# Performance work log

Hardware: AMD Instinct MI355X
Metric: run time of the kernel (lower is better)

## Reference

```python
import jax, jax.numpy as jnp
import numpy as np

B, T, D, H, O, E = 4, 2048, 1024, 2048, 1024, 8
EPS = 1e-12  # torch F.normalize p=1 eps


def setup_inputs() -> dict:
    key = jax.random.key(0)
    ks = jax.random.split(key, 8)
    s = lambda *dims: 1.0 / np.sqrt(dims[0])
    return {
        "x": jax.random.normal(ks[0], (B, T, D), dtype=jnp.float32),
        "num_experts_chosen": 2,
        "W_gate": jax.random.normal(ks[1], (D, E), dtype=jnp.float32) * s(D),
        "b_gate": jnp.zeros((E,), dtype=jnp.float32),
        "W1": jax.random.normal(ks[2], (E, D, H), dtype=jnp.float32) * s(D),
        "b1": jnp.zeros((E, H), dtype=jnp.float32),
        "W2": jax.random.normal(ks[3], (E, H, O), dtype=jnp.float32) * s(H),
        "b2": jnp.zeros((E, O), dtype=jnp.float32),
    }


def reference(x, num_experts_chosen, W_gate, b_gate, W1, b1, W2, b2):
    # Router: softmax over experts -> [b, t, E]
    gating = jax.nn.softmax(jnp.einsum("btd,de->bte", x, W_gate) + b_gate, axis=-1)

    # Top-k mask (scatter of ones at top-k indices), then L1 renormalize
    _, topk_idx = jax.lax.top_k(gating, num_experts_chosen)  # [b, t, k]
    mask = jax.nn.one_hot(topk_idx, E, dtype=gating.dtype).sum(axis=-2)  # [b, t, E]
    g = gating * mask
    g = g / jnp.maximum(jnp.sum(jnp.abs(g), axis=-1, keepdims=True), EPS)

    # Dense compute of ALL experts (faithful to original), eval-mode dropout = identity
    h = jax.nn.relu(jnp.einsum("btd,edh->bteh", x, W1) + b1)  # [b, t, E, H]
    eo = jnp.einsum("bteh,eho->bteo", h, W2) + b2              # [b, t, E, O]

    # Weighted combine over experts
    return jnp.einsum("bte,bteo->bto", g, eo)
```

## Files before the change

kernel.cpp:

```cpp
#include <hip/hip_runtime.h>
#include <hip/hip_bf16.h>

typedef unsigned short u16;
typedef __attribute__((ext_vector_type(8))) short short8;
typedef __attribute__((ext_vector_type(4))) float floatx4;

#define NB 4
#define NT 2048
#define ND 1024
#define NH 2048
#define NO 1024
#define NE 8
#define NTOK (NB * NT)

#define BM 128
#define BN 128
#define BK 32

__device__ __forceinline__ u16 f2bf(float f) {
  __hip_bfloat16 h = __float2bfloat16(f);
  return *reinterpret_cast<u16*>(&h);
}

__device__ __forceinline__ float bf2f(unsigned u) {
  return __uint_as_float(u << 16);
}

__device__ __forceinline__ void async16(const u16* g, u16* l) {
  __builtin_amdgcn_global_load_lds(
      (const __attribute__((address_space(1))) void*)g,
      (__attribute__((address_space(3))) void*)l, 16, 0, 0);
}

__global__ __launch_bounds__(256) void transpose_cvt(
    const float* __restrict__ in, u16* __restrict__ out, int R, int C) {
  __shared__ float tile[64][65];
  int e = blockIdx.z;
  in  += (size_t)e * R * C;
  out += (size_t)e * R * C;
  int c0 = blockIdx.x * 64, r0 = blockIdx.y * 64;
  int t = threadIdx.x;
#pragma unroll
  for (int i = 0; i < 4; ++i) {
    int idx = t + i * 256;
    int r = idx >> 4, cq = idx & 15;
    float4 v = *(const float4*)&in[(size_t)(r0 + r) * C + c0 + cq * 4];
    tile[r][cq * 4 + 0] = v.x; tile[r][cq * 4 + 1] = v.y;
    tile[r][cq * 4 + 2] = v.z; tile[r][cq * 4 + 3] = v.w;
  }
  __syncthreads();
#pragma unroll
  for (int i = 0; i < 4; ++i) {
    int idx = t + i * 256;
    int c = idx >> 4, rq = idx & 15;
    uint2 p;
    p.x = (unsigned)f2bf(tile[rq * 4 + 0][c]) | ((unsigned)f2bf(tile[rq * 4 + 1][c]) << 16);
    p.y = (unsigned)f2bf(tile[rq * 4 + 2][c]) | ((unsigned)f2bf(tile[rq * 4 + 3][c]) << 16);
    *(uint2*)&out[(size_t)(c0 + c) * R + r0 + rq * 4] = p;
  }
}

__global__ __launch_bounds__(256) void router_kernel(
    const float* __restrict__ x, const float* __restrict__ Wg,
    const float* __restrict__ bg, u16* __restrict__ xbf,
    int* __restrict__ counts, int* __restrict__ entries,
    float* __restrict__ wts) {
  int t = threadIdx.x;
  int tok = blockIdx.x * 16 + (t >> 4);
  int l16 = t & 15;

  float acc[8] = {};
  const float* xrow = x + (size_t)tok * ND;
  u16* xbrow = xbf + (size_t)tok * ND;
#pragma unroll
  for (int i = 0; i < 16; ++i) {
    int d0 = l16 * 4 + i * 64;
    float4 xv = *(const float4*)&xrow[d0];
    uint2 p;
    p.x = (unsigned)f2bf(xv.x) | ((unsigned)f2bf(xv.y) << 16);
    p.y = (unsigned)f2bf(xv.z) | ((unsigned)f2bf(xv.w) << 16);
    *(uint2*)&xbrow[d0] = p;
    const float* wr = Wg + (size_t)d0 * NE;
#pragma unroll
    for (int j = 0; j < 4; ++j) {
      float xs = (j == 0) ? xv.x : (j == 1) ? xv.y : (j == 2) ? xv.z : xv.w;
      float4 w0 = *(const float4*)&wr[j * NE];
      float4 w1 = *(const float4*)&wr[j * NE + 4];
      acc[0] += xs * w0.x; acc[1] += xs * w0.y;
      acc[2] += xs * w0.z; acc[3] += xs * w0.w;
      acc[4] += xs * w1.x; acc[5] += xs * w1.y;
      acc[6] += xs * w1.z; acc[7] += xs * w1.w;
    }
  }
#pragma unroll
  for (int off = 8; off; off >>= 1)
#pragma unroll
    for (int k = 0; k < 8; ++k) acc[k] += __shfl_down(acc[k], off, 16);

  if (l16 == 0) {
    float best = -1e30f, second = -1e30f;
    int e0 = 0, e1 = 0;
#pragma unroll
    for (int i = 0; i < NE; ++i) {
      float L = acc[i] + bg[i];
      if (L > best) { second = best; e1 = e0; best = L; e0 = i; }
      else if (L > second) { second = L; e1 = i; }
    }
    float p1 = __expf(second - best);
    float inv = 1.f / (1.f + p1);
    int pos0 = atomicAdd(&counts[e0], 1);
    entries[e0 * NTOK + pos0] = tok * 2;      wts[e0 * NTOK + pos0] = inv;
    int pos1 = atomicAdd(&counts[e1], 1);
    entries[e1 * NTOK + pos1] = tok * 2 + 1;  wts[e1 * NTOK + pos1] = p1 * inv;
  }
}

__global__ __launch_bounds__(256) void gemm1_kernel(
    const u16* __restrict__ xbf, const u16* __restrict__ w1t,
    const float* __restrict__ b1, const int* __restrict__ counts,
    const int* __restrict__ entries, u16* __restrict__ hbuf) {
  int b = blockIdx.x;
  int e = b & 7;
  int r = b >> 3;
  int m0 = (r >> 4) * BM;
  int n0 = (r & 15) * BN;
  int cnt = counts[e];
  if (m0 >= cnt) return;
  int rem = cnt - m0; if (rem > BM) rem = BM;

  __shared__ u16 As[BM * BK];
  __shared__ u16 Bs[BN * BK];
  __shared__ int ent_s[BM];

  int t = threadIdx.x;
  if (t < BM) ent_s[t] = (t < rem) ? entries[e * NTOK + m0 + t] : entries[e * NTOK];
  __syncthreads();

  int lane = t & 63, wv = t >> 6;
  int r0s = wv * 32 + (lane >> 2);
  int r1s = r0s + 16;
  int pg0 = ((lane & 3) ^ (r0s & 3)) * 8;
  int pg1 = ((lane & 3) ^ (r1s & 3)) * 8;
  const u16* gA0 = xbf + (size_t)(ent_s[r0s] >> 1) * ND + pg0;
  const u16* gA1 = xbf + (size_t)(ent_s[r1s] >> 1) * ND + pg1;
  const u16* Bbase = w1t + (size_t)e * NH * ND + (size_t)n0 * ND;
  const u16* gB0 = Bbase + (size_t)r0s * ND + pg0;
  const u16* gB1 = Bbase + (size_t)r1s * ND + pg1;
  u16* lA0 = As + (wv * 32) * BK;
  u16* lA1 = As + (wv * 32 + 16) * BK;
  u16* lB0 = Bs + (wv * 32) * BK;
  u16* lB1 = Bs + (wv * 32 + 16) * BK;

  int waveM = (wv >> 1) * 64, waveN = (wv & 1) * 64;
  int rA = lane & 15, quad = lane >> 4;
  int xq = (quad ^ (rA & 3)) * 8;
  const short8* aP[4]; const short8* bP[4];
#pragma unroll
  for (int i = 0; i < 4; ++i) {
    aP[i] = (const short8*)&As[(waveM + i * 16 + rA) * BK + xq];
    bP[i] = (const short8*)&Bs[(waveN + i * 16 + rA) * BK + xq];
  }

  floatx4 acc[4][4] = {};
  for (int k0 = 0; k0 < ND; k0 += BK) {
    async16(gA0 + k0, lA0);
    async16(gA1 + k0, lA1);
    async16(gB0 + k0, lB0);
    async16(gB1 + k0, lB1);
    __syncthreads();
    short8 a[4], b[4];
#pragma unroll
    for (int i = 0; i < 4; ++i) { a[i] = *aP[i]; b[i] = *bP[i]; }
#pragma unroll
    for (int i = 0; i < 4; ++i)
#pragma unroll
      for (int j = 0; j < 4; ++j)
        acc[i][j] = __builtin_amdgcn_mfma_f32_16x16x32_bf16(a[i], b[j], acc[i][j], 0, 0, 0);
    __syncthreads();
  }

#pragma unroll
  for (int i = 0; i < 4; ++i)
#pragma unroll
    for (int rr = 0; rr < 4; ++rr) {
      int lm = waveM + i * 16 + quad * 4 + rr;
      if (lm >= rem) continue;
      int ent = ent_s[lm];
      u16* dst = hbuf + (size_t)ent * NH + n0;
#pragma unroll
      for (int j = 0; j < 4; ++j) {
        int col = waveN + j * 16 + rA;
        float v = acc[i][j][rr] + b1[e * NH + n0 + col];
        dst[col] = f2bf(fmaxf(v, 0.f));
      }
    }
}

__global__ __launch_bounds__(256) void gemm2_kernel(
    const u16* __restrict__ hbuf, const u16* __restrict__ w2t,
    const float* __restrict__ b2, const int* __restrict__ counts,
    const int* __restrict__ entries, const float* __restrict__ wts,
    u16* __restrict__ eo) {
  int b = blockIdx.x;
  int e = b & 7;
  int r = b >> 3;
  int m0 = (r >> 3) * BM;
  int n0 = (r & 7) * BN;
  int cnt = counts[e];
  if (m0 >= cnt) return;
  int rem = cnt - m0; if (rem > BM) rem = BM;

  __shared__ u16 As[BM * BK];
  __shared__ u16 Bs[BN * BK];
  __shared__ int ent_s[BM];
  __shared__ float w_s[BM];

  int t = threadIdx.x;
  if (t < BM) {
    int src = (t < rem) ? (e * NTOK + m0 + t) : (e * NTOK);
    ent_s[t] = entries[src];
    w_s[t] = wts[src];
  }
  __syncthreads();

  int lane = t & 63, wv = t >> 6;
  int r0s = wv * 32 + (lane >> 2);
  int r1s = r0s + 16;
  int pg0 = ((lane & 3) ^ (r0s & 3)) * 8;
  int pg1 = ((lane & 3) ^ (r1s & 3)) * 8;
  const u16* gA0 = hbuf + (size_t)ent_s[r0s] * NH + pg0;
  const u16* gA1 = hbuf + (size_t)ent_s[r1s] * NH + pg1;
  const u16* Bbase = w2t + (size_t)e * NO * NH + (size_t)n0 * NH;
  const u16* gB0 = Bbase + (size_t)r0s * NH + pg0;
  const u16* gB1 = Bbase + (size_t)r1s * NH + pg1;
  u16* lA0 = As + (wv * 32) * BK;
  u16* lA1 = As + (wv * 32 + 16) * BK;
  u16* lB0 = Bs + (wv * 32) * BK;
  u16* lB1 = Bs + (wv * 32 + 16) * BK;

  int waveM = (wv >> 1) * 64, waveN = (wv & 1) * 64;
  int rA = lane & 15, quad = lane >> 4;
  int xq = (quad ^ (rA & 3)) * 8;
  const short8* aP[4]; const short8* bP[4];
#pragma unroll
  for (int i = 0; i < 4; ++i) {
    aP[i] = (const short8*)&As[(waveM + i * 16 + rA) * BK + xq];
    bP[i] = (const short8*)&Bs[(waveN + i * 16 + rA) * BK + xq];
  }

  floatx4 acc[4][4] = {};
  for (int k0 = 0; k0 < NH; k0 += BK) {
    async16(gA0 + k0, lA0);
    async16(gA1 + k0, lA1);
    async16(gB0 + k0, lB0);
    async16(gB1 + k0, lB1);
    __syncthreads();
    short8 a[4], b[4];
#pragma unroll
    for (int i = 0; i < 4; ++i) { a[i] = *aP[i]; b[i] = *bP[i]; }
#pragma unroll
    for (int i = 0; i < 4; ++i)
#pragma unroll
      for (int j = 0; j < 4; ++j)
        acc[i][j] = __builtin_amdgcn_mfma_f32_16x16x32_bf16(a[i], b[j], acc[i][j], 0, 0, 0);
    __syncthreads();
  }

#pragma unroll
  for (int i = 0; i < 4; ++i)
#pragma unroll
    for (int rr = 0; rr < 4; ++rr) {
      int lm = waveM + i * 16 + quad * 4 + rr;
      if (lm >= rem) continue;
      int ent = ent_s[lm];
      float w = w_s[lm];
      u16* dst = eo + (size_t)ent * NO + n0;
#pragma unroll
      for (int j = 0; j < 4; ++j) {
        int col = waveN + j * 16 + rA;
        float v = (acc[i][j][rr] + b2[e * NO + n0 + col]) * w;
        dst[col] = f2bf(v);
      }
    }
}

__global__ __launch_bounds__(256) void combine_kernel(
    const u16* __restrict__ eo, float* __restrict__ out) {
  size_t idx = (size_t)blockIdx.x * 256 + threadIdx.x;
  size_t tok = idx >> 8;
  int oq = (int)(idx & 255) * 4;
  const u16* p0 = eo + (tok * 2) * NO + oq;
  const u16* p1 = p0 + NO;
  uint2 ua = *(const uint2*)p0;
  uint2 ub = *(const uint2*)p1;
  float4 o;
  o.x = bf2f(ua.x & 0xffff) + bf2f(ub.x & 0xffff);
  o.y = bf2f(ua.x >> 16)    + bf2f(ub.x >> 16);
  o.z = bf2f(ua.y & 0xffff) + bf2f(ub.y & 0xffff);
  o.w = bf2f(ua.y >> 16)    + bf2f(ub.y >> 16);
  *(float4*)&out[tok * NO + oq] = o;
}

extern "C" void kernel_launch(void* const* d_in, const int* in_sizes, int n_in,
                              void* d_out, int out_size, void* d_ws, size_t ws_size,
                              hipStream_t stream) {
  (void)in_sizes; (void)n_in; (void)out_size; (void)ws_size;
  const float* x  = (const float*)d_in[0];
  const float* Wg = (const float*)d_in[2];
  const float* bg = (const float*)d_in[3];
  const float* W1 = (const float*)d_in[4];
  const float* b1 = (const float*)d_in[5];
  const float* W2 = (const float*)d_in[6];
  const float* b2 = (const float*)d_in[7];
  float* out = (float*)d_out;

  char* ws = (char*)d_ws;
  size_t off = 0;
  int*   counts  = (int*)(ws + off);   off += 256;
  int*   entries = (int*)(ws + off);   off += (size_t)NE * NTOK * 4;
  float* wts     = (float*)(ws + off); off += (size_t)NE * NTOK * 4;
  u16*   xbf     = (u16*)(ws + off);   off += (size_t)NTOK * ND * 2;
  u16*   w1t     = (u16*)(ws + off);   off += (size_t)NE * NH * ND * 2;
  u16*   w2t     = (u16*)(ws + off);   off += (size_t)NE * NO * NH * 2;
  u16*   hbuf    = (u16*)(ws + off);   off += (size_t)NTOK * 2 * NH * 2;
  u16*   eo      = w1t;

  hipMemsetAsync(counts, 0, 256, stream);

  transpose_cvt<<<dim3(NH / 64, ND / 64, NE), 256, 0, stream>>>(W1, w1t, ND, NH);
  transpose_cvt<<<dim3(NO / 64, NH / 64, NE), 256, 0, stream>>>(W2, w2t, NH, NO);
  router_kernel<<<NTOK / 16, 256, 0, stream>>>(x, Wg, bg, xbf, counts, entries, wts);
  gemm1_kernel<<<NE * (NTOK / BM) * (NH / BN), 256, 0, stream>>>(xbf, w1t, b1, counts, entries, hbuf);
  gemm2_kernel<<<NE * (NTOK / BM) * (NO / BN), 256, 0, stream>>>(hbuf, w2t, b2, counts, entries, wts, eo);
  combine_kernel<<<(NTOK * NO / 4) / 256, 256, 0, stream>>>(eo, out);
}
```

Measured before the change: 487.3 us.

## Double GEMM K-tile with 8-way swizzle and batch router atomics per block

Raises the K tile of both expert GEMMs from 32 to 64, using an 8-chunk XOR swizzle for LDS staging and issuing two MFMA k-steps per barrier pair. This halves the number of barriers and global-to-LDS rounds per output tile, at the cost of twice the shared memory per block. The router now handles 32 tokens per block and aggregates expert assignments in shared memory. It then does one atomicAdd per expert per block on counters padded to separate cache lines, which cuts atomic contention in exchange for serial writes by 8 threads.

```diff
diff --git a/kernel.cpp b/kernel.cpp
--- a/kernel.cpp
+++ b/kernel.cpp
@@ -15,7 +15,7 @@
 
 #define BM 128
 #define BN 128
-#define BK 32
+#define BK 64
 
 __device__ __forceinline__ u16 f2bf(float f) {
   __hip_bfloat16 h = __float2bfloat16(f);
@@ -65,16 +65,19 @@
     const float* __restrict__ bg, u16* __restrict__ xbf,
     int* __restrict__ counts, int* __restrict__ entries,
     float* __restrict__ wts) {
+  __shared__ int   se0[32], se1[32];
+  __shared__ float sw0[32], sw1[32];
   int t = threadIdx.x;
-  int tok = blockIdx.x * 16 + (t >> 4);
-  int l16 = t & 15;
-
-  float acc[8] = {};
+  int tl = t >> 3;
+  int l8 = t & 7;
+  int tok = blockIdx.x * 32 + tl;
+
   const float* xrow = x + (size_t)tok * ND;
   u16* xbrow = xbf + (size_t)tok * ND;
-#pragma unroll
-  for (int i = 0; i < 16; ++i) {
-    int d0 = l16 * 4 + i * 64;
+  float acc[8] = {};
+#pragma unroll 4
+  for (int i = 0; i < 32; ++i) {
+    int d0 = l8 * 4 + i * 32;
     float4 xv = *(const float4*)&xrow[d0];
     uint2 p;
     p.x = (unsigned)f2bf(xv.x) | ((unsigned)f2bf(xv.y) << 16);
@@ -93,11 +96,11 @@
     }
   }
 #pragma unroll
-  for (int off = 8; off; off >>= 1)
-#pragma unroll
-    for (int k = 0; k < 8; ++k) acc[k] += __shfl_down(acc[k], off, 16);
-
-  if (l16 == 0) {
+  for (int off = 4; off; off >>= 1)
+#pragma unroll
+    for (int k = 0; k < 8; ++k) acc[k] += __shfl_down(acc[k], off, 8);
+
+  if (l8 == 0) {
     float best = -1e30f, second = -1e30f;
     int e0 = 0, e1 = 0;
 #pragma unroll
@@ -108,10 +111,22 @@
     }
     float p1 = __expf(second - best);
     float inv = 1.f / (1.f + p1);
-    int pos0 = atomicAdd(&counts[e0], 1);
-    entries[e0 * NTOK + pos0] = tok * 2;      wts[e0 * NTOK + pos0] = inv;
-    int pos1 = atomicAdd(&counts[e1], 1);
-    entries[e1 * NTOK + pos1] = tok * 2 + 1;  wts[e1 * NTOK + pos1] = p1 * inv;
+    se0[tl] = e0; se1[tl] = e1;
+    sw0[tl] = inv; sw1[tl] = p1 * inv;
+  }
+  __syncthreads();
+
+  if (t < NE) {
+    int e = t;
+    int c = 0;
+#pragma unroll
+    for (int k = 0; k < 32; ++k) c += (se0[k] == e) + (se1[k] == e);
+    int pos = atomicAdd(&counts[e * 32], c);
+    int base = blockIdx.x * 32;
+    for (int k = 0; k < 32; ++k) {
+      if (se0[k] == e) { entries[e * NTOK + pos] = (base + k) * 2;     wts[e * NTOK + pos] = sw0[k]; ++pos; }
+      if (se1[k] == e) { entries[e * NTOK + pos] = (base + k) * 2 + 1; wts[e * NTOK + pos] = sw1[k]; ++pos; }
+    }
   }
 }
 
@@ -124,7 +139,7 @@
   int r = b >> 3;
   int m0 = (r >> 4) * BM;
   int n0 = (r & 15) * BN;
-  int cnt = counts[e];
+  int cnt = counts[e * 32];
   if (m0 >= cnt) return;
   int rem = cnt - m0; if (rem > BM) rem = BM;
 
@@ -137,45 +152,53 @@
   __syncthreads();
 
   int lane = t & 63, wv = t >> 6;
-  int r0s = wv * 32 + (lane >> 2);
-  int r1s = r0s + 16;
-  int pg0 = ((lane & 3) ^ (r0s & 3)) * 8;
-  int pg1 = ((lane & 3) ^ (r1s & 3)) * 8;
-  const u16* gA0 = xbf + (size_t)(ent_s[r0s] >> 1) * ND + pg0;
-  const u16* gA1 = xbf + (size_t)(ent_s[r1s] >> 1) * ND + pg1;
+  int srow = lane >> 3;
+  int schunk = lane & 7;
+  int pg = (schunk ^ srow) * 8;
+
   const u16* Bbase = w1t + (size_t)e * NH * ND + (size_t)n0 * ND;
-  const u16* gB0 = Bbase + (size_t)r0s * ND + pg0;
-  const u16* gB1 = Bbase + (size_t)r1s * ND + pg1;
-  u16* lA0 = As + (wv * 32) * BK;
-  u16* lA1 = As + (wv * 32 + 16) * BK;
-  u16* lB0 = Bs + (wv * 32) * BK;
-  u16* lB1 = Bs + (wv * 32 + 16) * BK;
+  const u16* gA[4]; const u16* gB[4];
+  u16 *lA[4], *lB[4];
+#pragma unroll
+  for (int j = 0; j < 4; ++j) {
+    int rr = wv * 32 + j * 8 + srow;
+    gA[j] = xbf + (size_t)(ent_s[rr] >> 1) * ND + pg;
+    gB[j] = Bbase + (size_t)rr * ND + pg;
+    lA[j] = As + (wv * 32 + j * 8) * BK;
+    lB[j] = Bs + (wv * 32 + j * 8) * BK;
+  }
 
   int waveM = (wv >> 1) * 64, waveN = (wv & 1) * 64;
   int rA = lane & 15, quad = lane >> 4;
-  int xq = (quad ^ (rA & 3)) * 8;
-  const short8* aP[4]; const short8* bP[4];
-#pragma unroll
-  for (int i = 0; i < 4; ++i) {
-    aP[i] = (const short8*)&As[(waveM + i * 16 + rA) * BK + xq];
-    bP[i] = (const short8*)&Bs[(waveN + i * 16 + rA) * BK + xq];
-  }
+  const short8* aP[2][4]; const short8* bP[2][4];
+#pragma unroll
+  for (int kk = 0; kk < 2; ++kk)
+#pragma unroll
+    for (int i = 0; i < 4; ++i) {
+      int cA = ((kk * 4 + quad) ^ (rA & 7)) * 8;
+      aP[kk][i] = (const short8*)&As[(waveM + i * 16 + rA) * BK + cA];
+      bP[kk][i] = (const short8*)&Bs[(waveN + i * 16 + rA) * BK + cA];
+    }
 
   floatx4 acc[4][4] = {};
   for (int k0 = 0; k0 < ND; k0 += BK) {
-    async16(gA0 + k0, lA0);
-    async16(gA1 + k0, lA1);
-    async16(gB0 + k0, lB0);
-    async16(gB1 + k0, lB1);
+#pragma unroll
+    for (int j = 0; j < 4; ++j) async16(gA[j] + k0, lA[j]);
+#pragma unroll
+    for (int j = 0; j < 4; ++j) async16(gB[j] + k0, lB[j]);
     __syncthreads();
-    short8 a[4], b[4];
-#pragma unroll
-    for (int i = 0; i < 4; ++i) { a[i] = *aP[i]; b[i] = *bP[i]; }
-#pragma unroll
-    for (int i = 0; i < 4; ++i)
-#pragma unroll
-      for (int j = 0; j < 4; ++j)
-        acc[i][j] = __builtin_amdgcn_mfma_f32_16x16x32_bf16(a[i], b[j], acc[i][j], 0, 0, 0);
+    short8 a[2][4], bb[2][4];
+#pragma unroll
+    for (int kk = 0; kk < 2; ++kk)
+#pragma unroll
+      for (int i = 0; i < 4; ++i) { a[kk][i] = *aP[kk][i]; bb[kk][i] = *bP[kk][i]; }
+#pragma unroll
+    for (int kk = 0; kk < 2; ++kk)
+#pragma unroll
+      for (int i = 0; i < 4; ++i)
+#pragma unroll
+        for (int j = 0; j < 4; ++j)
+          acc[i][j] = __builtin_amdgcn_mfma_f32_16x16x32_bf16(a[kk][i], bb[kk][j], acc[i][j], 0, 0, 0);
     __syncthreads();
   }
 
@@ -206,7 +229,7 @@
   int r = b >> 3;
   int m0 = (r >> 3) * BM;
   int n0 = (r & 7) * BN;
-  int cnt = counts[e];
+  int cnt = counts[e * 32];
   if (m0 >= cnt) return;
   int rem = cnt - m0; if (rem > BM) rem = BM;
 
@@ -224,45 +247,53 @@
   __syncthreads();
 
   int lane = t & 63, wv = t >> 6;
-  int r0s = wv * 32 + (lane >> 2);
-  int r1s = r0s + 16;
-  int pg0 = ((lane & 3) ^ (r0s & 3)) * 8;
-  int pg1 = ((lane & 3) ^ (r1s & 3)) * 8;
-  const u16* gA0 = hbuf + (size_t)ent_s[r0s] * NH + pg0;
-  const u16* gA1 = hbuf + (size_t)ent_s[r1s] * NH + pg1;
+  int srow = lane >> 3;
+  int schunk = lane & 7;
+  int pg = (schunk ^ srow) * 8;
+
   const u16* Bbase = w2t + (size_t)e * NO * NH + (size_t)n0 * NH;
-  const u16* gB0 = Bbase + (size_t)r0s * NH + pg0;
-  const u16* gB1 = Bbase + (size_t)r1s * NH + pg1;
-  u16* lA0 = As + (wv * 32) * BK;
-  u16* lA1 = As + (wv * 32 + 16) * BK;
-  u16* lB0 = Bs + (wv * 32) * BK;
-  u16* lB1 = Bs + (wv * 32 + 16) * BK;
+  const u16* gA[4]; const u16* gB[4];
+  u16 *lA[4], *lB[4];
+#pragma unroll
+  for (int j = 0; j < 4; ++j) {
+    int rr = wv * 32 + j * 8 + srow;
+    gA[j] = hbuf + (size_t)ent_s[rr] * NH + pg;
+    gB[j] = Bbase + (size_t)rr * NH + pg;
+    lA[j] = As + (wv * 32 + j * 8) * BK;
+    lB[j] = Bs + (wv * 32 + j * 8) * BK;
+  }
 
   int waveM = (wv >> 1) * 64, waveN = (wv & 1) * 64;
   int rA = lane & 15, quad = lane >> 4;
-  int xq = (quad ^ (rA & 3)) * 8;
-  const short8* aP[4]; const short8* bP[4];
-#pragma unroll
-  for (int i = 0; i < 4; ++i) {
-    aP[i] = (const short8*)&As[(waveM + i * 16 + rA) * BK + xq];
-    bP[i] = (const short8*)&Bs[(waveN + i * 16 + rA) * BK + xq];
-  }
+  const short8* aP[2][4]; const short8* bP[2][4];
+#pragma unroll
+  for (int kk = 0; kk < 2; ++kk)
+#pragma unroll
+    for (int i = 0; i < 4; ++i) {
+      int cA = ((kk * 4 + quad) ^ (rA & 7)) * 8;
+      aP[kk][i] = (const short8*)&As[(waveM + i * 16 + rA) * BK + cA];
+      bP[kk][i] = (const short8*)&Bs[(waveN + i * 16 + rA) * BK + cA];
+    }
 
   floatx4 acc[4][4] = {};
   for (int k0 = 0; k0 < NH; k0 += BK) {
-    async16(gA0 + k0, lA0);
-    async16(gA1 + k0, lA1);
-    async16(gB0 + k0, lB0);
-    async16(gB1 + k0, lB1);
+#pragma unroll
+    for (int j = 0; j < 4; ++j) async16(gA[j] + k0, lA[j]);
+#pragma unroll
+    for (int j = 0; j < 4; ++j) async16(gB[j] + k0, lB[j]);
     __syncthreads();
-    short8 a[4], b[4];
-#pragma unroll
-    for (int i = 0; i < 4; ++i) { a[i] = *aP[i]; b[i] = *bP[i]; }
-#pragma unroll
-    for (int i = 0; i < 4; ++i)
-#pragma unroll
-      for (int j = 0; j < 4; ++j)
-        acc[i][j] = __builtin_amdgcn_mfma_f32_16x16x32_bf16(a[i], b[j], acc[i][j], 0, 0, 0);
+    short8 a[2][4], bb[2][4];
+#pragma unroll
+    for (int kk = 0; kk < 2; ++kk)
+#pragma unroll
+      for (int i = 0; i < 4; ++i) { a[kk][i] = *aP[kk][i]; bb[kk][i] = *bP[kk][i]; }
+#pragma unroll
+    for (int kk = 0; kk < 2; ++kk)
+#pragma unroll
+      for (int i = 0; i < 4; ++i)
+#pragma unroll
+        for (int j = 0; j < 4; ++j)
+          acc[i][j] = __builtin_amdgcn_mfma_f32_16x16x32_bf16(a[kk][i], bb[kk][j], acc[i][j], 0, 0, 0);
     __syncthreads();
   }
 
@@ -316,7 +347,7 @@
 
   char* ws = (char*)d_ws;
   size_t off = 0;
-  int*   counts  = (int*)(ws + off);   off += 256;
+  int*   counts  = (int*)(ws + off);   off += NE * 32 * 4;
   int*   entries = (int*)(ws + off);   off += (size_t)NE * NTOK * 4;
   float* wts     = (float*)(ws + off); off += (size_t)NE * NTOK * 4;
   u16*   xbf     = (u16*)(ws + off);   off += (size_t)NTOK * ND * 2;
@@ -325,11 +356,11 @@
   u16*   hbuf    = (u16*)(ws + off);   off += (size_t)NTOK * 2 * NH * 2;
   u16*   eo      = w1t;
 
-  hipMemsetAsync(counts, 0, 256, stream);
+  hipMemsetAsync(counts, 0, NE * 32 * 4, stream);
 
   transpose_cvt<<<dim3(NH / 64, ND / 64, NE), 256, 0, stream>>>(W1, w1t, ND, NH);
   transpose_cvt<<<dim3(NO / 64, NH / 64, NE), 256, 0, stream>>>(W2, w2t, NH, NO);
-  router_kernel<<<NTOK / 16, 256, 0, stream>>>(x, Wg, bg, xbf, counts, entries, wts);
+  router_kernel<<<NTOK / 32, 256, 0, stream>>>(x, Wg, bg, xbf, counts, entries, wts);
   gemm1_kernel<<<NE * (NTOK / BM) * (NH / BN), 256, 0, stream>>>(xbf, w1t, b1, counts, entries, hbuf);
   gemm2_kernel<<<NE * (NTOK / BM) * (NO / BN), 256, 0, stream>>>(hbuf, w2t, b2, counts, entries, wts, eo);
   combine_kernel<<<(NTOK * NO / 4) / 256, 256, 0, stream>>>(eo, out);
```

Result: faster. 469.0 us (-3.7%).

## Aggregate router atomics per block, pad counters, and change LDS swizzle

Applied to the files above, without the earlier changes.

The router now handles 32 tokens per block with 8 lanes per token. Instead of one atomic per token-expert pair, each block tallies its picks per expert in shared memory and reserves all slots with a single atomicAdd. Expert counters are padded to separate 128-byte lines to avoid contention between experts. The GEMM kernels also switch the LDS XOR swizzle to use row>>1, aiming to reduce bank conflicts on the 16-byte fragment reads. Fewer lanes per token means more serial work per thread in the router.

```diff
diff --git a/kernel.cpp b/kernel.cpp
--- a/kernel.cpp
+++ b/kernel.cpp
@@ -65,16 +65,19 @@
     const float* __restrict__ bg, u16* __restrict__ xbf,
     int* __restrict__ counts, int* __restrict__ entries,
     float* __restrict__ wts) {
+  __shared__ int   se0[32], se1[32];
+  __shared__ float sw0[32], sw1[32];
   int t = threadIdx.x;
-  int tok = blockIdx.x * 16 + (t >> 4);
-  int l16 = t & 15;
-
-  float acc[8] = {};
+  int tl = t >> 3;
+  int l8 = t & 7;
+  int tok = blockIdx.x * 32 + tl;
+
   const float* xrow = x + (size_t)tok * ND;
   u16* xbrow = xbf + (size_t)tok * ND;
-#pragma unroll
-  for (int i = 0; i < 16; ++i) {
-    int d0 = l16 * 4 + i * 64;
+  float acc[8] = {};
+#pragma unroll 4
+  for (int i = 0; i < 32; ++i) {
+    int d0 = l8 * 4 + i * 32;
     float4 xv = *(const float4*)&xrow[d0];
     uint2 p;
     p.x = (unsigned)f2bf(xv.x) | ((unsigned)f2bf(xv.y) << 16);
@@ -93,11 +96,11 @@
     }
   }
 #pragma unroll
-  for (int off = 8; off; off >>= 1)
-#pragma unroll
-    for (int k = 0; k < 8; ++k) acc[k] += __shfl_down(acc[k], off, 16);
-
-  if (l16 == 0) {
+  for (int off = 4; off; off >>= 1)
+#pragma unroll
+    for (int k = 0; k < 8; ++k) acc[k] += __shfl_down(acc[k], off, 8);
+
+  if (l8 == 0) {
     float best = -1e30f, second = -1e30f;
     int e0 = 0, e1 = 0;
 #pragma unroll
@@ -108,10 +111,22 @@
     }
     float p1 = __expf(second - best);
     float inv = 1.f / (1.f + p1);
-    int pos0 = atomicAdd(&counts[e0], 1);
-    entries[e0 * NTOK + pos0] = tok * 2;      wts[e0 * NTOK + pos0] = inv;
-    int pos1 = atomicAdd(&counts[e1], 1);
-    entries[e1 * NTOK + pos1] = tok * 2 + 1;  wts[e1 * NTOK + pos1] = p1 * inv;
+    se0[tl] = e0; se1[tl] = e1;
+    sw0[tl] = inv; sw1[tl] = p1 * inv;
+  }
+  __syncthreads();
+
+  if (t < NE) {
+    int e = t;
+    int c = 0;
+#pragma unroll
+    for (int k = 0; k < 32; ++k) c += (se0[k] == e) + (se1[k] == e);
+    int pos = atomicAdd(&counts[e * 32], c);
+    int base = blockIdx.x * 32;
+    for (int k = 0; k < 32; ++k) {
+      if (se0[k] == e) { entries[e * NTOK + pos] = (base + k) * 2;     wts[e * NTOK + pos] = sw0[k]; ++pos; }
+      if (se1[k] == e) { entries[e * NTOK + pos] = (base + k) * 2 + 1; wts[e * NTOK + pos] = sw1[k]; ++pos; }
+    }
   }
 }
 
@@ -124,7 +139,7 @@
   int r = b >> 3;
   int m0 = (r >> 4) * BM;
   int n0 = (r & 15) * BN;
-  int cnt = counts[e];
+  int cnt = counts[e * 32];
   if (m0 >= cnt) return;
   int rem = cnt - m0; if (rem > BM) rem = BM;
 
@@ -137,15 +152,14 @@
   __syncthreads();
 
   int lane = t & 63, wv = t >> 6;
-  int r0s = wv * 32 + (lane >> 2);
-  int r1s = r0s + 16;
-  int pg0 = ((lane & 3) ^ (r0s & 3)) * 8;
-  int pg1 = ((lane & 3) ^ (r1s & 3)) * 8;
-  const u16* gA0 = xbf + (size_t)(ent_s[r0s] >> 1) * ND + pg0;
-  const u16* gA1 = xbf + (size_t)(ent_s[r1s] >> 1) * ND + pg1;
+  int rl0 = wv * 32 + (lane >> 2);
+  int rl1 = rl0 + 16;
+  int pg = (((lane & 3) ^ ((rl0 >> 1) & 3))) * 8;
+  const u16* gA0 = xbf + (size_t)(ent_s[rl0] >> 1) * ND + pg;
+  const u16* gA1 = xbf + (size_t)(ent_s[rl1] >> 1) * ND + pg;
   const u16* Bbase = w1t + (size_t)e * NH * ND + (size_t)n0 * ND;
-  const u16* gB0 = Bbase + (size_t)r0s * ND + pg0;
-  const u16* gB1 = Bbase + (size_t)r1s * ND + pg1;
+  const u16* gB0 = Bbase + (size_t)rl0 * ND + pg;
+  const u16* gB1 = Bbase + (size_t)rl1 * ND + pg;
   u16* lA0 = As + (wv * 32) * BK;
   u16* lA1 = As + (wv * 32 + 16) * BK;
   u16* lB0 = Bs + (wv * 32) * BK;
@@ -153,12 +167,12 @@
 
   int waveM = (wv >> 1) * 64, waveN = (wv & 1) * 64;
   int rA = lane & 15, quad = lane >> 4;
-  int xq = (quad ^ (rA & 3)) * 8;
+  int cR = (quad ^ ((rA >> 1) & 3)) * 8;
   const short8* aP[4]; const short8* bP[4];
 #pragma unroll
   for (int i = 0; i < 4; ++i) {
-    aP[i] = (const short8*)&As[(waveM + i * 16 + rA) * BK + xq];
-    bP[i] = (const short8*)&Bs[(waveN + i * 16 + rA) * BK + xq];
+    aP[i] = (const short8*)&As[(waveM + i * 16 + rA) * BK + cR];
+    bP[i] = (const short8*)&Bs[(waveN + i * 16 + rA) * BK + cR];
   }
 
   floatx4 acc[4][4] = {};
@@ -168,14 +182,14 @@
     async16(gB0 + k0, lB0);
     async16(gB1 + k0, lB1);
     __syncthreads();
-    short8 a[4], b[4];
-#pragma unroll
-    for (int i = 0; i < 4; ++i) { a[i] = *aP[i]; b[i] = *bP[i]; }
+    short8 a[4], bb[4];
+#pragma unroll
+    for (int i = 0; i < 4; ++i) { a[i] = *aP[i]; bb[i] = *bP[i]; }
 #pragma unroll
     for (int i = 0; i < 4; ++i)
 #pragma unroll
       for (int j = 0; j < 4; ++j)
-        acc[i][j] = __builtin_amdgcn_mfma_f32_16x16x32_bf16(a[i], b[j], acc[i][j], 0, 0, 0);
+        acc[i][j] = __builtin_amdgcn_mfma_f32_16x16x32_bf16(a[i], bb[j], acc[i][j], 0, 0, 0);
     __syncthreads();
   }
 
@@ -206,7 +220,7 @@
   int r = b >> 3;
   int m0 = (r >> 3) * BM;
   int n0 = (r & 7) * BN;
-  int cnt = counts[e];
+  int cnt = counts[e * 32];
   if (m0 >= cnt) return;
   int rem = cnt - m0; if (rem > BM) rem = BM;
 
@@ -224,15 +238,14 @@
   __syncthreads();
 
   int lane = t & 63, wv = t >> 6;
-  int r0s = wv * 32 + (lane >> 2);
-  int r1s = r0s + 16;
-  int pg0 = ((lane & 3) ^ (r0s & 3)) * 8;
-  int pg1 = ((lane & 3) ^ (r1s & 3)) * 8;
-  const u16* gA0 = hbuf + (size_t)ent_s[r0s] * NH + pg0;
-  const u16* gA1 = hbuf + (size_t)ent_s[r1s] * NH + pg1;
+  int rl0 = wv * 32 + (lane >> 2);
+  int rl1 = rl0 + 16;
+  int pg = (((lane & 3) ^ ((rl0 >> 1) & 3))) * 8;
+  const u16* gA0 = hbuf + (size_t)ent_s[rl0] * NH + pg;
+  const u16* gA1 = hbuf + (size_t)ent_s[rl1] * NH + pg;
   const u16* Bbase = w2t + (size_t)e * NO * NH + (size_t)n0 * NH;
-  const u16* gB0 = Bbase + (size_t)r0s * NH + pg0;
-  const u16* gB1 = Bbase + (size_t)r1s * NH + pg1;
+  const u16* gB0 = Bbase + (size_t)rl0 * NH + pg;
+  const u16* gB1 = Bbase + (size_t)rl1 * NH + pg;
   u16* lA0 = As + (wv * 32) * BK;
   u16* lA1 = As + (wv * 32 + 16) * BK;
   u16* lB0 = Bs + (wv * 32) * BK;
@@ -240,12 +253,12 @@
 
   int waveM = (wv >> 1) * 64, waveN = (wv & 1) * 64;
   int rA = lane & 15, quad = lane >> 4;
-  int xq = (quad ^ (rA & 3)) * 8;
+  int cR = (quad ^ ((rA >> 1) & 3)) * 8;
   const short8* aP[4]; const short8* bP[4];
 #pragma unroll
   for (int i = 0; i < 4; ++i) {
-    aP[i] = (const short8*)&As[(waveM + i * 16 + rA) * BK + xq];
-    bP[i] = (const short8*)&Bs[(waveN + i * 16 + rA) * BK + xq];
+    aP[i] = (const short8*)&As[(waveM + i * 16 + rA) * BK + cR];
+    bP[i] = (const short8*)&Bs[(waveN + i * 16 + rA) * BK + cR];
   }
 
   floatx4 acc[4][4] = {};
@@ -255,14 +268,14 @@
     async16(gB0 + k0, lB0);
     async16(gB1 + k0, lB1);
     __syncthreads();
-    short8 a[4], b[4];
-#pragma unroll
-    for (int i = 0; i < 4; ++i) { a[i] = *aP[i]; b[i] = *bP[i]; }
+    short8 a[4], bb[4];
+#pragma unroll
+    for (int i = 0; i < 4; ++i) { a[i] = *aP[i]; bb[i] = *bP[i]; }
 #pragma unroll
     for (int i = 0; i < 4; ++i)
 #pragma unroll
       for (int j = 0; j < 4; ++j)
-        acc[i][j] = __builtin_amdgcn_mfma_f32_16x16x32_bf16(a[i], b[j], acc[i][j], 0, 0, 0);
+        acc[i][j] = __builtin_amdgcn_mfma_f32_16x16x32_bf16(a[i], bb[j], acc[i][j], 0, 0, 0);
     __syncthreads();
   }
 
@@ -316,7 +329,7 @@
 
   char* ws = (char*)d_ws;
   size_t off = 0;
-  int*   counts  = (int*)(ws + off);   off += 256;
+  int*   counts  = (int*)(ws + off);   off += NE * 32 * 4;
   int*   entries = (int*)(ws + off);   off += (size_t)NE * NTOK * 4;
   float* wts     = (float*)(ws + off); off += (size_t)NE * NTOK * 4;
   u16*   xbf     = (u16*)(ws + off);   off += (size_t)NTOK * ND * 2;
@@ -325,11 +338,11 @@
   u16*   hbuf    = (u16*)(ws + off);   off += (size_t)NTOK * 2 * NH * 2;
   u16*   eo      = w1t;
 
-  hipMemsetAsync(counts, 0, 256, stream);
+  hipMemsetAsync(counts, 0, NE * 32 * 4, stream);
 
   transpose_cvt<<<dim3(NH / 64, ND / 64, NE), 256, 0, stream>>>(W1, w1t, ND, NH);
   transpose_cvt<<<dim3(NO / 64, NH / 64, NE), 256, 0, stream>>>(W2, w2t, NH, NO);
-  router_kernel<<<NTOK / 16, 256, 0, stream>>>(x, Wg, bg, xbf, counts, entries, wts);
+  router_kernel<<<NTOK / 32, 256, 0, stream>>>(x, Wg, bg, xbf, counts, entries, wts);
   gemm1_kernel<<<NE * (NTOK / BM) * (NH / BN), 256, 0, stream>>>(xbf, w1t, b1, counts, entries, hbuf);
   gemm2_kernel<<<NE * (NTOK / BM) * (NO / BN), 256, 0, stream>>>(hbuf, w2t, b2, counts, entries, wts, eo);
   combine_kernel<<<(NTOK * NO / 4) / 256, 256, 0, stream>>>(eo, out);
```

New measurement: 437.9 us. 10.1% less time.
